# Kernel optimization log

Measured on AMD Instinct MI355X. Metric: run time of the kernel, lower is better.

The kernel has to match this reference:

```python
import jax, jax.numpy as jnp
from jax import lax
import numpy as np

THRESHOLD = 0.8
SECONDARY = 0.6
SECONDARY_WEIGHT = 0.5
BN_EPS = 1e-5


def _conv_relu_pool(x, W, b):
    # x: [B,C,H,W], W: [O,I,3,3]
    y = lax.conv_general_dilated(x, W, window_strides=(1, 1), padding='SAME',
                                 dimension_numbers=('NCHW', 'OIHW', 'NCHW'))
    y = y + b[None, :, None, None]
    y = jax.nn.relu(y)
    return lax.reduce_window(y, -jnp.inf, lax.max, (1, 1, 2, 2), (1, 1, 2, 2), 'VALID')


def setup_inputs() -> dict:
    key = jax.random.key(0)
    ks = jax.random.split(key, 12)
    B, H, W = 1024, 64, 64
    d0, d1, d2 = 4096, 1024, 256  # qnn_arch
    inp = {}
    inp['x'] = jax.random.normal(ks[0], (B, 1, H, W), dtype=jnp.float32)
    # conv params (kaiming-ish scaling)
    inp['cw1'] = jax.random.normal(ks[1], (8, 1, 3, 3), jnp.float32) * (1.0 / np.sqrt(1 * 9))
    inp['cb1'] = jax.random.normal(ks[2], (8,), jnp.float32) * 0.01
    inp['cw2'] = jax.random.normal(ks[3], (16, 8, 3, 3), jnp.float32) * (1.0 / np.sqrt(8 * 9))
    inp['cb2'] = jax.random.normal(ks[4], (16,), jnp.float32) * 0.01
    # linear layers of the 'graph QNN'
    inp['w1'] = jax.random.normal(ks[5], (d1, d0), jnp.float32) * (1.0 / np.sqrt(d0))
    inp['b1'] = jax.random.normal(ks[6], (d1,), jnp.float32) * 0.01
    inp['w2'] = jax.random.normal(ks[7], (d2, d1), jnp.float32) * (1.0 / np.sqrt(d1))
    inp['b2'] = jax.random.normal(ks[8], (d2,), jnp.float32) * 0.01
    # BatchNorm1d affine params
    inp['gamma'] = jnp.ones((d2,), jnp.float32)
    inp['beta'] = jnp.zeros((d2,), jnp.float32)
    return inp


def reference(x, cw1, cb1, cw2, cb2, w1, b1, w2, b2, gamma, beta):
    B = x.shape[0]
    # CNN feature extractor
    feat = _conv_relu_pool(x, cw1, cb1)
    feat = _conv_relu_pool(feat, cw2, cb2)
    flat = feat.reshape(B, -1)                      # [B, 4096]
    # graph-QNN layers with tanh
    h1 = jnp.tanh(flat @ w1.T + b1)                 # [B, 1024]
    last = jnp.tanh(h1 @ w2.T + b2)                 # [B, 256]
    # fidelity adjacency: vectorized normalize + Gram + squared cosine
    norms = jnp.linalg.norm(last, axis=1, keepdims=True)  # [B,1]
    nrm = last / (norms + 1e-12)
    fid = (nrm @ nrm.T) ** 2                        # [B, B]
    adj = jnp.where(fid >= THRESHOLD, 1.0,
                    jnp.where(fid >= SECONDARY, SECONDARY_WEIGHT, 0.0))
    adj = adj * (1.0 - jnp.eye(B, dtype=adj.dtype))  # no self-edges
    # BatchNorm1d (training mode: batch statistics, biased variance)
    mean = jnp.mean(last, axis=0)
    var = jnp.mean((last - mean) ** 2, axis=0)
    out = (last - mean) / jnp.sqrt(var + BN_EPS) * gamma + beta
    return out, adj
```

## Files before the change

kernel.cpp:

```cpp
#include <hip/hip_runtime.h>
#include <hip/hip_bf16.h>
#include <math.h>


__global__ __launch_bounds__(256) void conv_fused(
    const float* __restrict__ x,
    const float* __restrict__ cw1, const float* __restrict__ cb1,
    const float* __restrict__ cw2, const float* __restrict__ cb2,
    float* __restrict__ flat) {
  __shared__ float sX[66 * 66];
  __shared__ float sF[8 * 34 * 34];
  __shared__ float sW1[72];
  __shared__ float sW2[1152];
  __shared__ float sB1[8];
  __shared__ float sB2[16];

  const int b = blockIdx.x;
  const int t = threadIdx.x;

  for (int i = t; i < 66 * 66; i += 256) sX[i] = 0.0f;
  for (int i = t; i < 8 * 34 * 34; i += 256) sF[i] = 0.0f;
  if (t < 72) sW1[t] = cw1[t];
  for (int i = t; i < 1152; i += 256) sW2[i] = cw2[i];
  if (t < 8)  sB1[t] = cb1[t];
  if (t < 16) sB2[t] = cb2[t];
  __syncthreads();

  const float* xb = x + (size_t)b * 4096;
  for (int i = t; i < 4096; i += 256)
    sX[((i >> 6) + 1) * 66 + (i & 63) + 1] = xb[i];
  __syncthreads();

  for (int p = t; p < 8192; p += 256) {
    const int ch = p >> 10, pos = p & 1023;
    const int py1 = pos >> 5, px1 = pos & 31;
    double best = -1e300;
#pragma unroll
    for (int dy = 0; dy < 2; ++dy) {
#pragma unroll
      for (int dx = 0; dx < 2; ++dx) {
        const int y = 2 * py1 + dy, xx = 2 * px1 + dx;
        double s = 0.0;
#pragma unroll
        for (int ky = 0; ky < 3; ++ky)
#pragma unroll
          for (int kx = 0; kx < 3; ++kx)
            s = fma((double)sX[(y + ky) * 66 + xx + kx],
                    (double)sW1[ch * 9 + ky * 3 + kx], s);
        best = fmax(best, s);
      }
    }
    sF[ch * 1156 + (py1 + 1) * 34 + px1 + 1] =
        (float)fmax(best + (double)sB1[ch], 0.0);
  }
  __syncthreads();

  const int py = t >> 4, px = t & 15;
  for (int oh = 0; oh < 2; ++oh) {
    double acc[8][4];
#pragma unroll
    for (int o = 0; o < 8; ++o)
#pragma unroll
      for (int q = 0; q < 4; ++q) acc[o][q] = 0.0;

#pragma unroll
    for (int ic = 0; ic < 8; ++ic) {
      double r[4][4];
#pragma unroll
      for (int iy = 0; iy < 4; ++iy)
#pragma unroll
        for (int ix = 0; ix < 4; ++ix)
          r[iy][ix] = (double)sF[ic * 1156 + (2 * py + iy) * 34 + 2 * px + ix];
#pragma unroll
      for (int o = 0; o < 8; ++o) {
        const float* w = &sW2[(oh * 8 + o) * 72 + ic * 9];
        double w9[9];
#pragma unroll
        for (int k = 0; k < 9; ++k) w9[k] = (double)w[k];
#pragma unroll
        for (int dy = 0; dy < 2; ++dy)
#pragma unroll
          for (int dx = 0; dx < 2; ++dx) {
            double s = acc[o][dy * 2 + dx];
#pragma unroll
            for (int ky = 0; ky < 3; ++ky)
#pragma unroll
              for (int kx = 0; kx < 3; ++kx)
                s = fma(r[dy + ky][dx + kx], w9[ky * 3 + kx], s);
            acc[o][dy * 2 + dx] = s;
          }
      }
    }

    float* ob = flat + (size_t)b * 4096 + py * 16 + px;
#pragma unroll
    for (int o = 0; o < 8; ++o) {
      const int oc = oh * 8 + o;
      double best =
          fmax(fmax(acc[o][0], acc[o][1]), fmax(acc[o][2], acc[o][3]));
      ob[oc * 256] = (float)fmax(best + (double)sB2[oc], 0.0);
    }
  }
}

__global__ __launch_bounds__(256) void gemm_nt_f64_partial(
    const float* __restrict__ A, const float* __restrict__ B,
    double* __restrict__ P, int M, int N, int K, int Kc) {
  __shared__ double As[16][66];
  __shared__ double Bs[16][66];

  const int t = threadIdx.x;
  const int n0 = blockIdx.x * 64;
  const int m0 = blockIdx.y * 64;
  const int s  = blockIdx.z;
  const int kb = s * Kc;
  const int lm = t >> 2;
  const int lk4 = (t & 3) * 4;
  const int ty = t >> 4;
  const int tx = t & 15;

  double acc[4][4];
#pragma unroll
  for (int i = 0; i < 4; ++i)
#pragma unroll
    for (int j = 0; j < 4; ++j) acc[i][j] = 0.0;

  for (int k0 = kb; k0 < kb + Kc; k0 += 16) {
    const float4 av = *(const float4*)&A[(size_t)(m0 + lm) * K + k0 + lk4];
    const float4 bv = *(const float4*)&B[(size_t)(n0 + lm) * K + k0 + lk4];
    __syncthreads();
    As[lk4 + 0][lm] = (double)av.x; As[lk4 + 1][lm] = (double)av.y;
    As[lk4 + 2][lm] = (double)av.z; As[lk4 + 3][lm] = (double)av.w;
    Bs[lk4 + 0][lm] = (double)bv.x; Bs[lk4 + 1][lm] = (double)bv.y;
    Bs[lk4 + 2][lm] = (double)bv.z; Bs[lk4 + 3][lm] = (double)bv.w;
    __syncthreads();
#pragma unroll
    for (int k = 0; k < 16; ++k) {
      const double2 a01 = *(const double2*)&As[k][2 * ty];
      const double2 a23 = *(const double2*)&As[k][32 + 2 * ty];
      const double2 b01 = *(const double2*)&Bs[k][2 * tx];
      const double2 b23 = *(const double2*)&Bs[k][32 + 2 * tx];
      const double ar[4] = {a01.x, a01.y, a23.x, a23.y};
      const double br[4] = {b01.x, b01.y, b23.x, b23.y};
#pragma unroll
      for (int i = 0; i < 4; ++i)
#pragma unroll
        for (int j = 0; j < 4; ++j)
          acc[i][j] = fma(ar[i], br[j], acc[i][j]);
    }
  }

  double* Pp = P + (size_t)s * M * N;
  const int rows[4] = {m0 + 2 * ty, m0 + 2 * ty + 1,
                       m0 + 32 + 2 * ty, m0 + 32 + 2 * ty + 1};
  const int c0 = n0 + 2 * tx, c1 = n0 + 32 + 2 * tx;
#pragma unroll
  for (int i = 0; i < 4; ++i) {
    *(double2*)&Pp[(size_t)rows[i] * N + c0] =
        make_double2(acc[i][0], acc[i][1]);
    *(double2*)&Pp[(size_t)rows[i] * N + c1] =
        make_double2(acc[i][2], acc[i][3]);
  }
}

__global__ __launch_bounds__(256) void reduce_tanh(
    const double* __restrict__ P, int S, const float* __restrict__ bias,
    float* __restrict__ C, int N, int total) {
  const int idx = blockIdx.x * 256 + threadIdx.x;
  if (idx >= total) return;
  double sum = 0.0;
  for (int s = 0; s < S; ++s) sum += P[(size_t)s * total + idx];
  const float zg = (float)sum;
  const float z = zg + bias[idx % N];
  C[idx] = (float)tanh((double)z);
}

__global__ __launch_bounds__(256) void reduce_adj(
    const double* __restrict__ P, int S, float* __restrict__ adj, int N) {
  const int idx = blockIdx.x * 256 + threadIdx.x;
  const int total = N * N;
  if (idx >= total) return;
  double sum = 0.0;
  for (int s = 0; s < S; ++s) sum += P[(size_t)s * total + idx];
  const float g = (float)sum;
  const float fid = g * g;
  float v = (fid >= 0.8f) ? 1.0f : ((fid >= 0.6f) ? 0.5f : 0.0f);
  if (idx / N == idx % N) v = 0.0f;
  adj[idx] = v;
}

__global__ __launch_bounds__(256) void rownorm(
    const float* __restrict__ last, float* __restrict__ nrm) {
  const int b = blockIdx.x;
  const int t = threadIdx.x;
  const float v = last[(size_t)b * 256 + t];
  const float sq = v * v;
  double s = (double)sq;
#pragma unroll
  for (int o = 32; o > 0; o >>= 1) s += __shfl_down(s, o);
  __shared__ double red[4];
  if ((t & 63) == 0) red[t >> 6] = s;
  __syncthreads();
  const double total = red[0] + red[1] + red[2] + red[3];
  const float s32 = (float)total;
  const float den = sqrtf(s32) + 1e-12f;
  nrm[(size_t)b * 256 + t] = v / den;
}

__global__ __launch_bounds__(256) void bn_stats(
    const float* __restrict__ last, const float* __restrict__ gamma,
    const float* __restrict__ beta, float* __restrict__ out) {
  const int j = blockIdx.x;
  const int t = threadIdx.x;
  double v[4];
  double s = 0.0;
#pragma unroll
  for (int i = 0; i < 4; ++i) {
    v[i] = (double)last[(size_t)(i * 256 + t) * 256 + j];
    s += v[i];
  }
#pragma unroll
  for (int o = 32; o > 0; o >>= 1) s += __shfl_down(s, o);
  __shared__ double red[4];
  if ((t & 63) == 0) red[t >> 6] = s;
  __syncthreads();
  const double mean = (red[0] + red[1] + red[2] + red[3]) * (1.0 / 1024.0);
  double q = 0.0;
#pragma unroll
  for (int i = 0; i < 4; ++i) {
    const double d = v[i] - mean;
    q += d * d;
  }
#pragma unroll
  for (int o = 32; o > 0; o >>= 1) q += __shfl_down(q, o);
  __syncthreads();
  if ((t & 63) == 0) red[t >> 6] = q;
  __syncthreads();
  const double var = (red[0] + red[1] + red[2] + red[3]) * (1.0 / 1024.0);
  const double g = (double)gamma[j] / sqrt(var + 1e-5);
  const double be = (double)beta[j];
#pragma unroll
  for (int i = 0; i < 4; ++i)
    out[(size_t)(i * 256 + t) * 256 + j] = (float)((v[i] - mean) * g + be);
}

extern "C" void kernel_launch(void* const* d_in, const int* in_sizes, int n_in,
                              void* d_out, int out_size, void* d_ws,
                              size_t ws_size, hipStream_t stream) {
  const float* x     = (const float*)d_in[0];
  const float* cw1   = (const float*)d_in[1];
  const float* cb1   = (const float*)d_in[2];
  const float* cw2   = (const float*)d_in[3];
  const float* cb2   = (const float*)d_in[4];
  const float* w1    = (const float*)d_in[5];
  const float* b1    = (const float*)d_in[6];
  const float* w2    = (const float*)d_in[7];
  const float* b2    = (const float*)d_in[8];
  const float* gamma = (const float*)d_in[9];
  const float* beta  = (const float*)d_in[10];

  float* outp = (float*)d_out;
  float* adj  = outp + 1024 * 256;

  float* ws   = (float*)d_ws;
  float* flat = ws;
  float* h1   = ws + 4194304;
  float* last = ws + 5242880;
  float* nrm  = ws + 5505024;
  double* part = (double*)(ws + 5767168);

  const size_t base = 5767168ull * 4ull;
  const int S1 = (ws_size >= base + 4ull * 1024 * 1024 * 8) ? 4 : 2;

  conv_fused<<<1024, 256, 0, stream>>>(x, cw1, cb1, cw2, cb2, flat);

  gemm_nt_f64_partial<<<dim3(16, 16, S1), 256, 0, stream>>>(
      flat, w1, part, 1024, 1024, 4096, 4096 / S1);
  reduce_tanh<<<4096, 256, 0, stream>>>(part, S1, b1, h1, 1024, 1024 * 1024);

  gemm_nt_f64_partial<<<dim3(4, 16, 4), 256, 0, stream>>>(
      h1, w2, part, 1024, 256, 1024, 256);
  reduce_tanh<<<1024, 256, 0, stream>>>(part, 4, b2, last, 256, 1024 * 256);

  rownorm<<<1024, 256, 0, stream>>>(last, nrm);

  gemm_nt_f64_partial<<<dim3(16, 16, 2), 256, 0, stream>>>(
      nrm, nrm, part, 1024, 1024, 256, 128);
  reduce_adj<<<4096, 256, 0, stream>>>(part, 2, adj, 1024);

  bn_stats<<<256, 256, 0, stream>>>(last, gamma, beta, outp);
}
```

Before: 452.3 us.

## Split conv into two kernels, enlarge GEMM tile to 128x64, raise split-K

The fused conv kernel is replaced by two kernels. conv1 computes four pooled outputs per thread from a register window, and conv2 processes output channels in pairs to cut register pressure, with a global intermediate stored in the partial buffer. The fp64 GEMM tile grows to 128x64 so each thread holds 8x4 accumulators, which raises compute reuse per shared-memory load. Split-K factors go up when the workspace allows, giving more parallel blocks at the cost of more partial-sum traffic in the reductions. The extra round-trip of the conv intermediate through global memory and the higher register use per GEMM thread could reduce occupancy.

```diff
diff --git a/kernel.cpp b/kernel.cpp
--- a/kernel.cpp
+++ b/kernel.cpp
@@ -2,6 +2,146 @@
 #include <hip/hip_bf16.h>
 #include <math.h>
 
+
+__global__ __launch_bounds__(256) void conv1_kernel(
+    const float* __restrict__ x, const float* __restrict__ cw1,
+    const float* __restrict__ cb1, float* __restrict__ feat1) {
+  __shared__ float sX[66 * 66];
+  __shared__ float sW1[72];
+  __shared__ float sB1[8];
+
+  const int b = blockIdx.x;
+  const int t = threadIdx.x;
+
+  for (int i = t; i < 66 * 66; i += 256) sX[i] = 0.0f;
+  if (t < 72) sW1[t] = cw1[t];
+  if (t < 8)  sB1[t] = cb1[t];
+  __syncthreads();
+
+  const float* xb = x + (size_t)b * 4096;
+  for (int i = t; i < 4096; i += 256)
+    sX[((i >> 6) + 1) * 66 + (i & 63) + 1] = xb[i];
+  __syncthreads();
+
+  for (int task = t; task < 2048; task += 256) {
+    const int ch = task >> 8;
+    const int rem = task & 255;
+    const int py = rem >> 3;
+    const int px0 = (rem & 7) * 4;
+
+    double w9[9];
+#pragma unroll
+    for (int k = 0; k < 9; ++k) w9[k] = (double)sW1[ch * 9 + k];
+
+    float reg[4][10];
+#pragma unroll
+    for (int r = 0; r < 4; ++r)
+#pragma unroll
+      for (int c = 0; c < 5; ++c) {
+        const float2 v =
+            *(const float2*)&sX[(2 * py + r) * 66 + 2 * px0 + 2 * c];
+        reg[r][2 * c] = v.x;
+        reg[r][2 * c + 1] = v.y;
+      }
+
+    float out4[4];
+#pragma unroll
+    for (int px = 0; px < 4; ++px) {
+      double best = -1e300;
+#pragma unroll
+      for (int dy = 0; dy < 2; ++dy) {
+#pragma unroll
+        for (int dx = 0; dx < 2; ++dx) {
+          double s = 0.0;
+#pragma unroll
+          for (int ky = 0; ky < 3; ++ky)
+#pragma unroll
+            for (int kx = 0; kx < 3; ++kx)
+              s = fma((double)reg[dy + ky][2 * px + dx + kx], w9[ky * 3 + kx],
+                      s);
+          best = fmax(best, s);
+        }
+      }
+      out4[px] = (float)fmax(best + (double)sB1[ch], 0.0);
+    }
+    *(float4*)&feat1[(size_t)b * 8192 + ch * 1024 + py * 32 + px0] =
+        make_float4(out4[0], out4[1], out4[2], out4[3]);
+  }
+}
+
+__global__ __launch_bounds__(256) void conv2_kernel(
+    const float* __restrict__ feat1, const float* __restrict__ cw2,
+    const float* __restrict__ cb2, float* __restrict__ flat) {
+  __shared__ float sF[8 * 34 * 34];
+  __shared__ float sW2[1152];
+  __shared__ float sB2[16];
+
+  const int b = blockIdx.x;
+  const int t = threadIdx.x;
+
+  for (int i = t; i < 8 * 34 * 34; i += 256) sF[i] = 0.0f;
+  for (int i = t; i < 1152; i += 256) sW2[i] = cw2[i];
+  if (t < 16) sB2[t] = cb2[t];
+  __syncthreads();
+
+  const float* fb = feat1 + (size_t)b * 8192;
+  for (int i = t; i < 8192; i += 256) {
+    const int ch = i >> 10, pos = i & 1023;
+    sF[ch * 1156 + ((pos >> 5) + 1) * 34 + (pos & 31) + 1] = fb[i];
+  }
+  __syncthreads();
+
+  const int py = t >> 4, px = t & 15;
+  float* ob = flat + (size_t)b * 4096 + py * 16 + px;
+
+  for (int pair = 0; pair < 8; ++pair) {
+    double acc[2][4];
+#pragma unroll
+    for (int o = 0; o < 2; ++o)
+#pragma unroll
+      for (int q = 0; q < 4; ++q) acc[o][q] = 0.0;
+
+#pragma unroll
+    for (int ic = 0; ic < 8; ++ic) {
+      double r[4][4];
+#pragma unroll
+      for (int iy = 0; iy < 4; ++iy) {
+        const float2 v0 =
+            *(const float2*)&sF[ic * 1156 + (2 * py + iy) * 34 + 2 * px];
+        const float2 v1 =
+            *(const float2*)&sF[ic * 1156 + (2 * py + iy) * 34 + 2 * px + 2];
+        r[iy][0] = (double)v0.x; r[iy][1] = (double)v0.y;
+        r[iy][2] = (double)v1.x; r[iy][3] = (double)v1.y;
+      }
+#pragma unroll
+      for (int o = 0; o < 2; ++o) {
+        const int oc = 2 * pair + o;
+        double w9[9];
+#pragma unroll
+        for (int k = 0; k < 9; ++k) w9[k] = (double)sW2[oc * 72 + ic * 9 + k];
+#pragma unroll
+        for (int dy = 0; dy < 2; ++dy)
+#pragma unroll
+          for (int dx = 0; dx < 2; ++dx) {
+            double s = acc[o][dy * 2 + dx];
+#pragma unroll
+            for (int ky = 0; ky < 3; ++ky)
+#pragma unroll
+              for (int kx = 0; kx < 3; ++kx)
+                s = fma(r[dy + ky][dx + kx], w9[ky * 3 + kx], s);
+            acc[o][dy * 2 + dx] = s;
+          }
+      }
+    }
+#pragma unroll
+    for (int o = 0; o < 2; ++o) {
+      const int oc = 2 * pair + o;
+      const double best =
+          fmax(fmax(acc[o][0], acc[o][1]), fmax(acc[o][2], acc[o][3]));
+      ob[oc * 256] = (float)fmax(best + (double)sB2[oc], 0.0);
+    }
+  }
+}
 
 __global__ __launch_bounds__(256) void conv_fused(
     const float* __restrict__ x,
@@ -36,7 +176,7 @@
     const int py1 = pos >> 5, px1 = pos & 31;
     double best = -1e300;
 #pragma unroll
-    for (int dy = 0; dy < 2; ++dy) {
+    for (int dy = 0; dy < 2; ++dy)
 #pragma unroll
       for (int dx = 0; dx < 2; ++dx) {
         const int y = 2 * py1 + dy, xx = 2 * px1 + dx;
@@ -49,7 +189,6 @@
                     (double)sW1[ch * 9 + ky * 3 + kx], s);
         best = fmax(best, s);
       }
-    }
     sF[ch * 1156 + (py1 + 1) * 34 + px1 + 1] =
         (float)fmax(best + (double)sB1[ch], 0.0);
   }
@@ -62,7 +201,6 @@
     for (int o = 0; o < 8; ++o)
 #pragma unroll
       for (int q = 0; q < 4; ++q) acc[o][q] = 0.0;
-
 #pragma unroll
     for (int ic = 0; ic < 8; ++ic) {
       double r[4][4];
@@ -91,7 +229,6 @@
           }
       }
     }
-
     float* ob = flat + (size_t)b * 4096 + py * 16 + px;
 #pragma unroll
     for (int o = 0; o < 8; ++o) {
@@ -103,47 +240,52 @@
   }
 }
 
-__global__ __launch_bounds__(256) void gemm_nt_f64_partial(
+__global__ __launch_bounds__(256) void gemm_nt_f64_v2(
     const float* __restrict__ A, const float* __restrict__ B,
     double* __restrict__ P, int M, int N, int K, int Kc) {
-  __shared__ double As[16][66];
+  __shared__ double As[16][130];
   __shared__ double Bs[16][66];
 
   const int t = threadIdx.x;
   const int n0 = blockIdx.x * 64;
-  const int m0 = blockIdx.y * 64;
+  const int m0 = blockIdx.y * 128;
   const int s  = blockIdx.z;
   const int kb = s * Kc;
-  const int lm = t >> 2;
-  const int lk4 = (t & 3) * 4;
+  const int rS = t >> 2;
+  const int cS = (t & 3) * 4;
   const int ty = t >> 4;
   const int tx = t & 15;
 
-  double acc[4][4];
-#pragma unroll
-  for (int i = 0; i < 4; ++i)
+  double acc[8][4];
+#pragma unroll
+  for (int i = 0; i < 8; ++i)
 #pragma unroll
     for (int j = 0; j < 4; ++j) acc[i][j] = 0.0;
 
   for (int k0 = kb; k0 < kb + Kc; k0 += 16) {
-    const float4 av = *(const float4*)&A[(size_t)(m0 + lm) * K + k0 + lk4];
-    const float4 bv = *(const float4*)&B[(size_t)(n0 + lm) * K + k0 + lk4];
+    const float4 aLo = *(const float4*)&A[(size_t)(m0 + rS) * K + k0 + cS];
+    const float4 aHi = *(const float4*)&A[(size_t)(m0 + 64 + rS) * K + k0 + cS];
+    const float4 bV  = *(const float4*)&B[(size_t)(n0 + rS) * K + k0 + cS];
     __syncthreads();
-    As[lk4 + 0][lm] = (double)av.x; As[lk4 + 1][lm] = (double)av.y;
-    As[lk4 + 2][lm] = (double)av.z; As[lk4 + 3][lm] = (double)av.w;
-    Bs[lk4 + 0][lm] = (double)bv.x; Bs[lk4 + 1][lm] = (double)bv.y;
-    Bs[lk4 + 2][lm] = (double)bv.z; Bs[lk4 + 3][lm] = (double)bv.w;
+    As[cS + 0][rS] = (double)aLo.x; As[cS + 1][rS] = (double)aLo.y;
+    As[cS + 2][rS] = (double)aLo.z; As[cS + 3][rS] = (double)aLo.w;
+    As[cS + 0][64 + rS] = (double)aHi.x; As[cS + 1][64 + rS] = (double)aHi.y;
+    As[cS + 2][64 + rS] = (double)aHi.z; As[cS + 3][64 + rS] = (double)aHi.w;
+    Bs[cS + 0][rS] = (double)bV.x; Bs[cS + 1][rS] = (double)bV.y;
+    Bs[cS + 2][rS] = (double)bV.z; Bs[cS + 3][rS] = (double)bV.w;
     __syncthreads();
 #pragma unroll
     for (int k = 0; k < 16; ++k) {
-      const double2 a01 = *(const double2*)&As[k][2 * ty];
-      const double2 a23 = *(const double2*)&As[k][32 + 2 * ty];
-      const double2 b01 = *(const double2*)&Bs[k][2 * tx];
-      const double2 b23 = *(const double2*)&Bs[k][32 + 2 * tx];
-      const double ar[4] = {a01.x, a01.y, a23.x, a23.y};
-      const double br[4] = {b01.x, b01.y, b23.x, b23.y};
-#pragma unroll
-      for (int i = 0; i < 4; ++i)
+      const double2 a0 = *(const double2*)&As[k][2 * ty];
+      const double2 a1 = *(const double2*)&As[k][32 + 2 * ty];
+      const double2 a2 = *(const double2*)&As[k][64 + 2 * ty];
+      const double2 a3 = *(const double2*)&As[k][96 + 2 * ty];
+      const double2 b0 = *(const double2*)&Bs[k][2 * tx];
+      const double2 b1 = *(const double2*)&Bs[k][32 + 2 * tx];
+      const double ar[8] = {a0.x, a0.y, a1.x, a1.y, a2.x, a2.y, a3.x, a3.y};
+      const double br[4] = {b0.x, b0.y, b1.x, b1.y};
+#pragma unroll
+      for (int i = 0; i < 8; ++i)
 #pragma unroll
         for (int j = 0; j < 4; ++j)
           acc[i][j] = fma(ar[i], br[j], acc[i][j]);
@@ -151,15 +293,12 @@
   }
 
   double* Pp = P + (size_t)s * M * N;
-  const int rows[4] = {m0 + 2 * ty, m0 + 2 * ty + 1,
-                       m0 + 32 + 2 * ty, m0 + 32 + 2 * ty + 1};
   const int c0 = n0 + 2 * tx, c1 = n0 + 32 + 2 * tx;
 #pragma unroll
-  for (int i = 0; i < 4; ++i) {
-    *(double2*)&Pp[(size_t)rows[i] * N + c0] =
-        make_double2(acc[i][0], acc[i][1]);
-    *(double2*)&Pp[(size_t)rows[i] * N + c1] =
-        make_double2(acc[i][2], acc[i][3]);
+  for (int i = 0; i < 8; ++i) {
+    const int row = m0 + (i >> 1) * 32 + 2 * ty + (i & 1);
+    *(double2*)&Pp[(size_t)row * N + c0] = make_double2(acc[i][0], acc[i][1]);
+    *(double2*)&Pp[(size_t)row * N + c1] = make_double2(acc[i][2], acc[i][3]);
   }
 }
 
@@ -268,23 +407,34 @@
   float* last = ws + 5242880;
   float* nrm  = ws + 5505024;
   double* part = (double*)(ws + 5767168);
-
-  const size_t base = 5767168ull * 4ull;
-  const int S1 = (ws_size >= base + 4ull * 1024 * 1024 * 8) ? 4 : 2;
-
-  conv_fused<<<1024, 256, 0, stream>>>(x, cw1, cb1, cw2, cb2, flat);
-
-  gemm_nt_f64_partial<<<dim3(16, 16, S1), 256, 0, stream>>>(
+  float* feat1 = (float*)part;
+
+  const size_t baseB = 5767168ull * 4ull;
+  int S1;
+  if (ws_size >= baseB + 8ull * 1024 * 1024 * 8) S1 = 8;
+  else if (ws_size >= baseB + 4ull * 1024 * 1024 * 8) S1 = 4;
+  else S1 = 2;
+  const int S2 = (S1 >= 4) ? 16 : 4;
+  const bool split_conv = (S1 >= 4);
+
+  if (split_conv) {
+    conv1_kernel<<<1024, 256, 0, stream>>>(x, cw1, cb1, feat1);
+    conv2_kernel<<<1024, 256, 0, stream>>>(feat1, cw2, cb2, flat);
+  } else {
+    conv_fused<<<1024, 256, 0, stream>>>(x, cw1, cb1, cw2, cb2, flat);
+  }
+
+  gemm_nt_f64_v2<<<dim3(16, 8, S1), 256, 0, stream>>>(
       flat, w1, part, 1024, 1024, 4096, 4096 / S1);
   reduce_tanh<<<4096, 256, 0, stream>>>(part, S1, b1, h1, 1024, 1024 * 1024);
 
-  gemm_nt_f64_partial<<<dim3(4, 16, 4), 256, 0, stream>>>(
-      h1, w2, part, 1024, 256, 1024, 256);
-  reduce_tanh<<<1024, 256, 0, stream>>>(part, 4, b2, last, 256, 1024 * 256);
+  gemm_nt_f64_v2<<<dim3(4, 8, S2), 256, 0, stream>>>(
+      h1, w2, part, 1024, 256, 1024, 1024 / S2);
+  reduce_tanh<<<1024, 256, 0, stream>>>(part, S2, b2, last, 256, 1024 * 256);
 
   rownorm<<<1024, 256, 0, stream>>>(last, nrm);
 
-  gemm_nt_f64_partial<<<dim3(16, 16, 2), 256, 0, stream>>>(
+  gemm_nt_f64_v2<<<dim3(16, 8, 2), 256, 0, stream>>>(
       nrm, nrm, part, 1024, 1024, 256, 128);
   reduce_adj<<<4096, 256, 0, stream>>>(part, 2, adj, 1024);
 
```

Result: slower. 532.3 us (+17.7%).
